# Kernel optimization log

Measured on AMD Instinct MI355X. Metric: run time of the kernel, lower is better.

## Reference

```python
import jax, jax.numpy as jnp
import numpy as np

E = 8          # num_global_experts
K = 2          # top-k
D = 1024       # model_dim
H = 4096       # hidden_size_per_expert
CAP_FACTOR = 1.0


def setup_inputs() -> dict:
    key = jax.random.key(0)
    ks = jax.random.split(key, 5)
    x = jax.random.normal(ks[0], (4, 2048, D), jnp.float32)
    gate_w = jax.random.normal(ks[1], (E, D), jnp.float32) * 0.02
    fc1_w = jax.random.normal(ks[2], (E, H, D), jnp.float32) * 0.02
    fc1_b = jnp.zeros((E, 1, H), jnp.float32)
    fc2_w = jax.random.normal(ks[3], (E, H, D), jnp.float32) * 0.02
    fc2_b = jnp.zeros((E, 1, D), jnp.float32)
    return {"x": x, "gate_w": gate_w, "fc1_w": fc1_w, "fc1_b": fc1_b,
            "fc2_w": fc2_w, "fc2_b": fc2_b}


def reference(x, gate_w, fc1_w, fc1_b, fc2_w, fc2_b):
    B, S, Dm = x.shape
    xf = x.reshape(-1, Dm)                       # [N, D] tokens
    N = xf.shape[0]
    cap = int(K * CAP_FACTOR * ((N + E - 1) // E))  # expert capacity

    # ---- gating (top-k softmax, normalized) ----
    logits = xf @ gate_w.T                       # [N, E]
    scores = jax.nn.softmax(logits, axis=-1)
    topv, topi = jax.lax.top_k(scores, K)        # [N, K]
    gates = topv / jnp.sum(topv, axis=-1, keepdims=True)

    # ---- per-slot locations within each expert (sequential over K slots) ----
    offset = jnp.zeros((E,), jnp.int32)
    locs = []
    for j in range(K):
        mask = jax.nn.one_hot(topi[:, j], E, dtype=jnp.int32)   # [N, E]
        loc_in = jnp.cumsum(mask, axis=0) - 1 + offset[None, :]
        locs.append(jnp.take_along_axis(loc_in, topi[:, j:j + 1], axis=1)[:, 0])
        offset = offset + mask.sum(axis=0)
    loc = jnp.stack(locs, axis=1)                # [N, K]
    valid = loc < cap                            # capacity-dropped tokens
    flat_idx = jnp.where(valid, topi * cap + loc, 0)   # [N, K]
    w = valid.astype(xf.dtype)

    # ---- dispatch (scatter tokens into [E, cap, D], postscore => unweighted) ----
    disp = jnp.zeros((E * cap, Dm), xf.dtype)
    disp = disp.at[flat_idx.reshape(-1)].add(
        (xf[:, None, :] * w[:, :, None]).reshape(-1, Dm))
    de = disp.reshape(E, cap, Dm)

    # ---- batched expert FFN: relu(x @ fc1^T + b1) @ fc2 + b2 ----
    h = jax.nn.relu(jnp.einsum('ecd,ehd->ech', de, fc1_w) + fc1_b)
    eo = jnp.einsum('ech,ehd->ecd', h, fc2_w) + fc2_b

    # ---- combine (gather + gate-weighted sum over K slots) ----
    gathered = eo.reshape(E * cap, Dm)[flat_idx]       # [N, K, D]
    out = jnp.sum(gathered * (gates * w)[:, :, None], axis=1)
    return out.reshape(B, S, Dm)
```

## Files before the change

### kernel.cpp

```cpp
#include <hip/hip_runtime.h>
#include <hip/hip_bf16.h>
#include <stdint.h>

#define NEXP 8
#define DM   1024
#define HID  4096
#define NTOK 8192
#define CAPS 2048

#define BM 256
#define BN 256
#define BK 64

typedef __attribute__((ext_vector_type(8))) short bh8_t;
typedef __attribute__((ext_vector_type(4))) float f32x4_t;
typedef unsigned short u16;

static __device__ __forceinline__ u16 f2bf(float f) {
    __hip_bfloat16 h = __float2bfloat16(f);
    return __builtin_bit_cast(u16, h);
}
static __device__ __forceinline__ float bf2f(u16 u) {
    unsigned int x = ((unsigned int)u) << 16;
    return __builtin_bit_cast(float, x);
}

#define FENCE asm volatile("" ::: "memory")
#define BAR   do { FENCE; __builtin_amdgcn_s_barrier(); FENCE; } while (0)
#define SB0   __builtin_amdgcn_sched_barrier(0)
#define MFMA(d, a, b) d = __builtin_amdgcn_mfma_f32_16x16x32_bf16(a, b, d, 0, 0, 0)

__global__ __launch_bounds__(256) void k_conv_bf16(const float* __restrict__ in,
                                                   u16* __restrict__ out, long n4) {
    long stride = (long)gridDim.x * 256;
    for (long i = (long)blockIdx.x * 256 + threadIdx.x; i < n4; i += stride) {
        float4 v = ((const float4*)in)[i];
        ushort4 o;
        o.x = f2bf(v.x); o.y = f2bf(v.y); o.z = f2bf(v.z); o.w = f2bf(v.w);
        ((ushort4*)out)[i] = o;
    }
}

__global__ __launch_bounds__(256) void k_transpose_w2(const float* __restrict__ in,
                                                      u16* __restrict__ out) {
    int e = blockIdx.z;
    const float* I = in + (long)e * HID * DM;
    u16* O = out + (long)e * DM * HID;
    __shared__ float t[64][65];
    int h0 = blockIdx.x * 64, d0 = blockIdx.y * 64;
    int tid = threadIdx.x;
    int r = tid >> 4, cw = (tid & 15) * 4;
    #pragma unroll
    for (int i = 0; i < 4; ++i) {
        float4 v = *(const float4*)(I + (long)(h0 + r + 16*i) * DM + d0 + cw);
        t[r + 16*i][cw]     = v.x;
        t[r + 16*i][cw + 1] = v.y;
        t[r + 16*i][cw + 2] = v.z;
        t[r + 16*i][cw + 3] = v.w;
    }
    __syncthreads();
    int dl = tid >> 2, hc = (tid & 3) * 16;
    bh8_t w0, w1;
    #pragma unroll
    for (int j = 0; j < 8; ++j) w0[j] = (short)f2bf(t[hc + j][dl]);
    #pragma unroll
    for (int j = 0; j < 8; ++j) w1[j] = (short)f2bf(t[hc + 8 + j][dl]);
    u16* o = O + (long)(d0 + dl) * HID + h0 + hc;
    *(bh8_t*)o = w0;
    *(bh8_t*)(o + 8) = w1;
}

__global__ __launch_bounds__(256) void k_gating(const float* __restrict__ x,
        const float* __restrict__ gw, int* __restrict__ topi, float* __restrict__ gates) {
    __shared__ float sg[NEXP][DM];
    int tid = threadIdx.x;
    for (int i = tid; i < NEXP*DM; i += 256) ((float*)sg)[i] = gw[i];
    __syncthreads();
    int lane = tid & 63, w = tid >> 6;
    long n = (long)blockIdx.x * 4 + w;
    const float* xr = x + n * DM;
    float acc[NEXP] = {};
    for (int i = 0; i < DM/64; ++i) {
        float xv = xr[lane + i*64];
        #pragma unroll
        for (int e = 0; e < NEXP; ++e) acc[e] += xv * sg[e][lane + i*64];
    }
    #pragma unroll
    for (int e = 0; e < NEXP; ++e)
        #pragma unroll
        for (int off = 32; off; off >>= 1) acc[e] += __shfl_xor(acc[e], off);
    if (lane == 0) {
        float mx = acc[0];
        #pragma unroll
        for (int e = 1; e < NEXP; ++e) mx = fmaxf(mx, acc[e]);
        float p[NEXP];
        #pragma unroll
        for (int e = 0; e < NEXP; ++e) p[e] = expf(acc[e] - mx);
        float v0 = p[0]; int i0 = 0;
        #pragma unroll
        for (int e = 1; e < NEXP; ++e) if (p[e] > v0) { v0 = p[e]; i0 = e; }
        float v1 = -1.f; int i1 = 0;
        #pragma unroll
        for (int e = 0; e < NEXP; ++e) if (e != i0 && p[e] > v1) { v1 = p[e]; i1 = e; }
        float tot = v0 + v1;
        topi[n*2]   = i0; topi[n*2+1] = i1;
        gates[n*2]  = v0 / tot; gates[n*2+1] = v1 / tot;
    }
}

__global__ __launch_bounds__(256) void k_locate(const int* __restrict__ topi,
                                                int* __restrict__ flat) {
    __shared__ int st[NTOK * 2];
    __shared__ int wsum[4];
    int tid = threadIdx.x, lane = tid & 63, w = tid >> 6;
    int4* st4 = (int4*)st;
    const int4* g4 = (const int4*)topi;
    for (int i = tid; i < NTOK * 2 / 4; i += 256) st4[i] = g4[i];
    __syncthreads();
    const int TPL = NTOK / 256;
    int base = tid * TPL;
    int offset[NEXP];
    #pragma unroll
    for (int e = 0; e < NEXP; ++e) offset[e] = 0;
    for (int j = 0; j < 2; ++j) {
        unsigned long long pk = 0;
        for (int t = 0; t < TPL; ++t) pk += 1ull << (8 * st[(base + t) * 2 + j]);
        int excl[NEXP];
        #pragma unroll
        for (int e = 0; e < NEXP; ++e) {
            int cnt = (int)((pk >> (8 * e)) & 0xff);
            int v = cnt;
            #pragma unroll
            for (int d = 1; d < 64; d <<= 1) {
                int o = __shfl_up(v, d);
                if (lane >= d) v += o;
            }
            if (lane == 63) wsum[w] = v;
            __syncthreads();
            int wb = 0;
            #pragma unroll
            for (int ww = 0; ww < 4; ++ww) if (ww < w) wb += wsum[ww];
            int tot = wsum[0] + wsum[1] + wsum[2] + wsum[3];
            excl[e] = v - cnt + wb + offset[e];
            offset[e] += tot;
            __syncthreads();
        }
        unsigned long long lo = 0, hi = 0;
        #pragma unroll
        for (int e = 0; e < 4; ++e)    lo |= (unsigned long long)(excl[e] & 0xffff) << (16*e);
        #pragma unroll
        for (int e = 4; e < NEXP; ++e) hi |= (unsigned long long)(excl[e] & 0xffff) << (16*(e-4));
        for (int t = 0; t < TPL; ++t) {
            int n = base + t;
            int e = st[n * 2 + j];
            int sh = 16 * (e & 3);
            int loc;
            if (e < 4) { loc = (int)((lo >> sh) & 0xffff); lo += 1ull << sh; }
            else       { loc = (int)((hi >> sh) & 0xffff); hi += 1ull << sh; }
            st[n * 2 + j] = (loc < CAPS) ? (e * CAPS + loc) : -1;
        }
        __syncthreads();
    }
    int4* f4 = (int4*)flat;
    for (int i = tid; i < NTOK * 2 / 4; i += 256) f4[i] = st4[i];
}

__global__ __launch_bounds__(256) void k_dispatch(const float* __restrict__ x,
        const int* __restrict__ flat, u16* __restrict__ disp) {
    long n = blockIdx.x;
    int tid = threadIdx.x;
    float4 v = *(const float4*)(x + n*DM + tid*4);
    ushort4 o; o.x = f2bf(v.x); o.y = f2bf(v.y); o.z = f2bf(v.z); o.w = f2bf(v.w);
    int f0 = flat[n*2], f1 = flat[n*2+1];
    if (f0 >= 0) *(ushort4*)(disp + (long)f0*DM + tid*4) = o;
    if (f1 >= 0) *(ushort4*)(disp + (long)f1*DM + tid*4) = o;
}

static __device__ __forceinline__ void stage_half(const u16* __restrict__ g, int ld,
                                                  u16* R, int wid, int lane) {
    int rlo = wid*8 + (lane >> 3);
    int cbe = ((lane & 7) ^ ((lane >> 3) & 7)) * 8;
    const u16* s0 = g + (long)rlo * ld + cbe;
    const u16* s1 = g + (long)(rlo + 64) * ld + cbe;
    u16* d0 = R + wid*512 + lane*8;
    u16* d1 = R + 4096 + wid*512 + lane*8;
    __builtin_amdgcn_global_load_lds((const __attribute__((address_space(1))) void*)s0,
        (__attribute__((address_space(3))) void*)d0, 16, 0, 0);
    __builtin_amdgcn_global_load_lds((const __attribute__((address_space(1))) void*)s1,
        (__attribute__((address_space(3))) void*)d1, 16, 0, 0);
}

template<int RELU>
__global__ __launch_bounds__(512, 2)
void k_gemm8(const u16* __restrict__ A, const u16* __restrict__ B,
             const float* __restrict__ bias, u16* __restrict__ C,
             int N, int K, long strA, long strB, long strBias, long strC)
{
    __shared__ u16 sm[2][2][2][8192];

    int gx = gridDim.x, gy = gridDim.y;
    int nwg = gx * gy * (int)gridDim.z;
    int lin = blockIdx.x + gx * (blockIdx.y + gy * blockIdx.z);
    int qq  = nwg >> 3;
    int swz = (lin & 7) * qq + (lin >> 3);
    int gxy = gx * gy;
    int bz = swz / gxy, rm = swz % gxy, by = rm / gx, bx = rm % gx;

    const float* bi = bias + (long)bz * strBias;
    u16* Ce = C + (long)bz * strC;

    long tm = (long)by * BM, tn = (long)bx * BN;
    const u16* Abase = A + (long)bz * strA + tm * (long)K;
    const u16* Bbase = B + (long)bz * strB + tn * (long)K;

    int tid = threadIdx.x, lane = tid & 63, wid = tid >> 6;
    int wr = wid >> 2, wc = wid & 3;

    int frow = lane & 15;
    int fc0 = (((lane >> 4) * 16)      ^ ((lane & 7) << 4)) >> 1;
    int fc1 = ((64 + (lane >> 4) * 16) ^ ((lane & 7) << 4)) >> 1;

    const int NT = K / BK;

    f32x4_t acc[8][4] = {};

    auto STG = [&](int buf, int ab, int half, int kt) {
        const u16* g = (ab ? Bbase : Abase) + (long)(half * 128) * K + (long)kt * BK;
        stage_half(g, K, &sm[buf][ab][half][0], wid, lane);
    };
    auto LDA = [&](int c, int mi, int kk) -> bh8_t {
        const u16* p = &sm[c][0][wr][0] + (mi * 16 + frow) * 64 + (kk ? fc1 : fc0);
        return *(const bh8_t*)p;
    };
    auto LDB = [&](int c, int ni, int kk) -> bh8_t {
        const u16* p = &sm[c][1][wc >> 1][0] + ((wc & 1) * 64 + ni * 16 + frow) * 64 + (kk ? fc1 : fc0);
        return *(const bh8_t*)p;
    };

    auto ktile = [&](int c, int kt, int s12, int s34, int vm) {
        bh8_t a0[4][2], a1[4][2], bf[4][2];
        #pragma unroll
        for (int mi = 0; mi < 4; ++mi) { a0[mi][0] = LDA(c, mi, 0); a0[mi][1] = LDA(c, mi, 1); }
        #pragma unroll
        for (int ni = 0; ni < 2; ++ni) { bf[ni][0] = LDB(c, ni, 0); bf[ni][1] = LDB(c, ni, 1); }
        if (s12) STG(c ^ 1, 0, 1, kt + 1);
        BAR;
        __builtin_amdgcn_s_setprio(1);
        #pragma unroll
        for (int mi = 0; mi < 4; ++mi)
            #pragma unroll
            for (int ni = 0; ni < 2; ++ni)
                #pragma unroll
                for (int kk = 0; kk < 2; ++kk) MFMA(acc[mi][ni], a0[mi][kk], bf[ni][kk]);
        __builtin_amdgcn_s_setprio(0); SB0; BAR;
        #pragma unroll
        for (int ni = 2; ni < 4; ++ni) { bf[ni][0] = LDB(c, ni, 0); bf[ni][1] = LDB(c, ni, 1); }
        if (s12) STG(c ^ 1, 1, 1, kt + 1);
        BAR;
        __builtin_amdgcn_s_setprio(1);
        #pragma unroll
        for (int mi = 0; mi < 4; ++mi)
            #pragma unroll
            for (int ni = 2; ni < 4; ++ni)
                #pragma unroll
                for (int kk = 0; kk < 2; ++kk) MFMA(acc[mi][ni], a0[mi][kk], bf[ni][kk]);
        __builtin_amdgcn_s_setprio(0); SB0; BAR;
        #pragma unroll
        for (int mi = 0; mi < 4; ++mi) { a1[mi][0] = LDA(c, mi + 4, 0); a1[mi][1] = LDA(c, mi + 4, 1); }
        if (s34) STG(c, 1, 0, kt + 2);
        BAR;
        __builtin_amdgcn_s_setprio(1);
        #pragma unroll
        for (int mi = 0; mi < 4; ++mi)
            #pragma unroll
            for (int ni = 0; ni < 2; ++ni)
                #pragma unroll
                for (int kk = 0; kk < 2; ++kk) MFMA(acc[mi + 4][ni], a1[mi][kk], bf[ni][kk]);
        __builtin_amdgcn_s_setprio(0); SB0; BAR;
        if (s34) STG(c, 0, 0, kt + 2);
        BAR;
        __builtin_amdgcn_s_setprio(1);
        #pragma unroll
        for (int mi = 0; mi < 4; ++mi)
            #pragma unroll
            for (int ni = 2; ni < 4; ++ni)
                #pragma unroll
                for (int kk = 0; kk < 2; ++kk) MFMA(acc[mi + 4][ni], a1[mi][kk], bf[ni][kk]);
        __builtin_amdgcn_s_setprio(0); SB0;
        if (vm == 4)      { asm volatile("s_waitcnt vmcnt(4)" ::: "memory"); }
        else if (vm == 0) { asm volatile("s_waitcnt vmcnt(0)" ::: "memory"); }
        BAR;
    };

    STG(0, 0, 0, 0); STG(0, 0, 1, 0); STG(0, 1, 0, 0); STG(0, 1, 1, 0);
    STG(1, 1, 0, 1); STG(1, 0, 0, 1);
    asm volatile("s_waitcnt vmcnt(4)" ::: "memory");
    BAR;

    int kt = 0;
    for (; kt < NT - 2; ++kt) ktile(kt & 1, kt, 1, 1, 4);
    ktile(kt & 1, kt, 1, 0, 0); ++kt;
    ktile(kt & 1, kt, 0, 0, -1);

    u16* wb = &sm[0][0][0][0] + wid * 8192;
    #pragma unroll
    for (int mi = 0; mi < 8; ++mi)
        #pragma unroll
        for (int ni = 0; ni < 4; ++ni) {
            float bv = bi[tn + wc * 64 + ni * 16 + (lane & 15)];
            #pragma unroll
            for (int r = 0; r < 4; ++r) {
                int row = mi * 16 + (lane >> 4) * 4 + r;
                int ce  = ni * 16 + (lane & 15);
                float v = acc[mi][ni][r] + bv;
                if (RELU) v = fmaxf(v, 0.f);
                wb[row * 64 + (ce ^ ((row & 7) << 3))] = f2bf(v);
            }
        }
    __syncthreads();
    long crow = tm + wr * 128;
    long ccol = tn + wc * 64 + (lane & 7) * 8;
    #pragma unroll
    for (int i = 0; i < 16; ++i) {
        int rr = i * 8 + (lane >> 3);
        bh8_t v = *(const bh8_t*)(wb + rr * 64 + (((lane & 7) * 8) ^ ((rr & 7) << 3)));
        *(bh8_t*)(Ce + (crow + rr) * N + ccol) = v;
    }
}

__global__ __launch_bounds__(256) void k_combine(const u16* __restrict__ eo,
        const int* __restrict__ flat, const float* __restrict__ gates,
        float* __restrict__ out) {
    long n = blockIdx.x;
    int tid = threadIdx.x;
    int f0 = flat[n*2], f1 = flat[n*2+1];
    float g0 = (f0 >= 0) ? gates[n*2]   : 0.f;
    float g1 = (f1 >= 0) ? gates[n*2+1] : 0.f;
    const u16* r0 = eo + (long)(f0 >= 0 ? f0 : 0) * DM;
    const u16* r1 = eo + (long)(f1 >= 0 ? f1 : 0) * DM;
    ushort4 a = *(const ushort4*)(r0 + tid*4);
    ushort4 b = *(const ushort4*)(r1 + tid*4);
    float4 o;
    o.x = g0*bf2f(a.x) + g1*bf2f(b.x);
    o.y = g0*bf2f(a.y) + g1*bf2f(b.y);
    o.z = g0*bf2f(a.z) + g1*bf2f(b.z);
    o.w = g0*bf2f(a.w) + g1*bf2f(b.w);
    *(float4*)(out + n*DM + tid*4) = o;
}

extern "C" void kernel_launch(void* const* d_in, const int* in_sizes, int n_in,
                              void* d_out, int out_size, void* d_ws, size_t ws_size,
                              hipStream_t stream) {
    const float* x    = (const float*)d_in[0];
    const float* gw   = (const float*)d_in[1];
    const float* fc1w = (const float*)d_in[2];
    const float* fc1b = (const float*)d_in[3];
    const float* fc2w = (const float*)d_in[4];
    const float* fc2b = (const float*)d_in[5];
    float* out = (float*)d_out;
    char* ws = (char*)d_ws;

    u16* disp = (u16*)(ws);
    u16* eo   = disp;
    u16* h    = (u16*)(ws + 33554432L);
    u16* w1b  = (u16*)(ws + 33554432L + 134217728L);
    u16* w2t  = (u16*)(ws + 33554432L + 134217728L + 67108864L);
    char* tail = ws + 33554432L + 134217728L + 67108864L + 67108864L;
    int*   topi  = (int*)tail;
    float* gates = (float*)(tail + 65536);
    int*   flat  = (int*)(tail + 131072);

    long n1 = (long)NEXP * HID * DM;

    k_conv_bf16<<<dim3(2048), 256, 0, stream>>>(fc1w, w1b, n1 / 4);
    k_transpose_w2<<<dim3(HID/64, DM/64, NEXP), 256, 0, stream>>>(fc2w, w2t);
    k_gating<<<dim3(NTOK/4), 256, 0, stream>>>(x, gw, topi, gates);
    k_locate<<<dim3(1), 256, 0, stream>>>(topi, flat);
    k_dispatch<<<dim3(NTOK), 256, 0, stream>>>(x, flat, disp);
    k_gemm8<1><<<dim3(HID/BN, CAPS/BM, NEXP), 512, 0, stream>>>(
        disp, w1b, fc1b, h, HID, DM,
        (long)CAPS*DM, (long)HID*DM, (long)HID, (long)CAPS*HID);
    k_gemm8<0><<<dim3(DM/BN, CAPS/BM, NEXP), 512, 0, stream>>>(
        h, w2t, fc2b, eo, DM, HID,
        (long)CAPS*HID, (long)DM*HID, (long)DM, (long)CAPS*DM);
    k_combine<<<dim3(NTOK), 256, 0, stream>>>(eo, flat, gates, out);
}
```

Measured before the change: 397.5 us.

## Interleave warp tile ownership across staged halves to pipeline loads finer

Remaps each wave's 128x64 output subtile so it spans both staged halves of A and B (64 rows from each A half, 32 columns from each B half). Each k-tile's four MFMA phases can then start on the first half-tile while the other halves are still loading. The prefetch order and the vmcnt waits are restaged with finer per-phase counts. The epilogue bias indexing and global store addressing are rewritten to match the new fragment mapping. The cost is more complex index math and a different LDS access pattern that may change bank behaviour.

```diff
diff --git a/kernel.cpp b/kernel.cpp
--- a/kernel.cpp
+++ b/kernel.cpp
@@ -29,6 +29,10 @@
 #define BAR   do { FENCE; __builtin_amdgcn_s_barrier(); FENCE; } while (0)
 #define SB0   __builtin_amdgcn_sched_barrier(0)
 #define MFMA(d, a, b) d = __builtin_amdgcn_mfma_f32_16x16x32_bf16(a, b, d, 0, 0, 0)
+#define WAITVM(n) do { if ((n) == 8) asm volatile("s_waitcnt vmcnt(8)" ::: "memory"); \
+    else if ((n) == 4) asm volatile("s_waitcnt vmcnt(4)" ::: "memory"); \
+    else if ((n) == 2) asm volatile("s_waitcnt vmcnt(2)" ::: "memory"); \
+    else if ((n) == 0) asm volatile("s_waitcnt vmcnt(0)" ::: "memory"); } while (0)
 
 __global__ __launch_bounds__(256) void k_conv_bf16(const float* __restrict__ in,
                                                    u16* __restrict__ out, long n4) {
@@ -228,21 +232,34 @@
         const u16* g = (ab ? Bbase : Abase) + (long)(half * 128) * K + (long)kt * BK;
         stage_half(g, K, &sm[buf][ab][half][0], wid, lane);
     };
-    auto LDA = [&](int c, int mi, int kk) -> bh8_t {
-        const u16* p = &sm[c][0][wr][0] + (mi * 16 + frow) * 64 + (kk ? fc1 : fc0);
+    auto LDA = [&](int c, int half, int mi, int kk) -> bh8_t {
+        const u16* p = &sm[c][0][half][0] + (wr * 64 + mi * 16 + frow) * 64 + (kk ? fc1 : fc0);
         return *(const bh8_t*)p;
     };
-    auto LDB = [&](int c, int ni, int kk) -> bh8_t {
-        const u16* p = &sm[c][1][wc >> 1][0] + ((wc & 1) * 64 + ni * 16 + frow) * 64 + (kk ? fc1 : fc0);
+    auto LDB = [&](int c, int half, int ni, int kk) -> bh8_t {
+        const u16* p = &sm[c][1][half][0] + (wc * 32 + ni * 16 + frow) * 64 + (kk ? fc1 : fc0);
         return *(const bh8_t*)p;
     };
 
-    auto ktile = [&](int c, int kt, int s12, int s34, int vm) {
-        bh8_t a0[4][2], a1[4][2], bf[4][2];
-        #pragma unroll
-        for (int mi = 0; mi < 4; ++mi) { a0[mi][0] = LDA(c, mi, 0); a0[mi][1] = LDA(c, mi, 1); }
-        #pragma unroll
-        for (int ni = 0; ni < 2; ++ni) { bf[ni][0] = LDB(c, ni, 0); bf[ni][1] = LDB(c, ni, 1); }
+    auto ktile = [&](int c, int kt, int s12, int s34, int vm1, int vm2, int vm4) {
+        bh8_t a0[4][2], a1[4][2], b0[2][2], b1[2][2];
+        #pragma unroll
+        for (int mi = 0; mi < 4; ++mi) { a0[mi][0] = LDA(c, 0, mi, 0); a0[mi][1] = LDA(c, 0, mi, 1); }
+        #pragma unroll
+        for (int ni = 0; ni < 2; ++ni) { b0[ni][0] = LDB(c, 0, ni, 0); b0[ni][1] = LDB(c, 0, ni, 1); }
+        if (s12) STG(c ^ 1, 1, 1, kt + 1);
+        BAR;
+        __builtin_amdgcn_s_setprio(1);
+        #pragma unroll
+        for (int mi = 0; mi < 4; ++mi)
+            #pragma unroll
+            for (int ni = 0; ni < 2; ++ni)
+                #pragma unroll
+                for (int kk = 0; kk < 2; ++kk) MFMA(acc[mi][ni], a0[mi][kk], b0[ni][kk]);
+        __builtin_amdgcn_s_setprio(0); SB0;
+        WAITVM(vm1); BAR;
+        #pragma unroll
+        for (int ni = 0; ni < 2; ++ni) { b1[ni][0] = LDB(c, 1, ni, 0); b1[ni][1] = LDB(c, 1, ni, 1); }
         if (s12) STG(c ^ 1, 0, 1, kt + 1);
         BAR;
         __builtin_amdgcn_s_setprio(1);
@@ -251,22 +268,21 @@
             #pragma unroll
             for (int ni = 0; ni < 2; ++ni)
                 #pragma unroll
-                for (int kk = 0; kk < 2; ++kk) MFMA(acc[mi][ni], a0[mi][kk], bf[ni][kk]);
-        __builtin_amdgcn_s_setprio(0); SB0; BAR;
-        #pragma unroll
-        for (int ni = 2; ni < 4; ++ni) { bf[ni][0] = LDB(c, ni, 0); bf[ni][1] = LDB(c, ni, 1); }
-        if (s12) STG(c ^ 1, 1, 1, kt + 1);
+                for (int kk = 0; kk < 2; ++kk) MFMA(acc[mi][2 + ni], a0[mi][kk], b1[ni][kk]);
+        __builtin_amdgcn_s_setprio(0); SB0;
+        WAITVM(vm2); BAR;
+        #pragma unroll
+        for (int mi = 0; mi < 4; ++mi) { a1[mi][0] = LDA(c, 1, mi, 0); a1[mi][1] = LDA(c, 1, mi, 1); }
+        if (s34) STG(c, 0, 0, kt + 2);
         BAR;
         __builtin_amdgcn_s_setprio(1);
         #pragma unroll
         for (int mi = 0; mi < 4; ++mi)
             #pragma unroll
-            for (int ni = 2; ni < 4; ++ni)
+            for (int ni = 0; ni < 2; ++ni)
                 #pragma unroll
-                for (int kk = 0; kk < 2; ++kk) MFMA(acc[mi][ni], a0[mi][kk], bf[ni][kk]);
+                for (int kk = 0; kk < 2; ++kk) MFMA(acc[4 + mi][ni], a1[mi][kk], b0[ni][kk]);
         __builtin_amdgcn_s_setprio(0); SB0; BAR;
-        #pragma unroll
-        for (int mi = 0; mi < 4; ++mi) { a1[mi][0] = LDA(c, mi + 4, 0); a1[mi][1] = LDA(c, mi + 4, 1); }
         if (s34) STG(c, 1, 0, kt + 2);
         BAR;
         __builtin_amdgcn_s_setprio(1);
@@ -275,39 +291,27 @@
             #pragma unroll
             for (int ni = 0; ni < 2; ++ni)
                 #pragma unroll
-                for (int kk = 0; kk < 2; ++kk) MFMA(acc[mi + 4][ni], a1[mi][kk], bf[ni][kk]);
-        __builtin_amdgcn_s_setprio(0); SB0; BAR;
-        if (s34) STG(c, 0, 0, kt + 2);
-        BAR;
-        __builtin_amdgcn_s_setprio(1);
-        #pragma unroll
-        for (int mi = 0; mi < 4; ++mi)
-            #pragma unroll
-            for (int ni = 2; ni < 4; ++ni)
-                #pragma unroll
-                for (int kk = 0; kk < 2; ++kk) MFMA(acc[mi + 4][ni], a1[mi][kk], bf[ni][kk]);
+                for (int kk = 0; kk < 2; ++kk) MFMA(acc[4 + mi][2 + ni], a1[mi][kk], b1[ni][kk]);
         __builtin_amdgcn_s_setprio(0); SB0;
-        if (vm == 4)      { asm volatile("s_waitcnt vmcnt(4)" ::: "memory"); }
-        else if (vm == 0) { asm volatile("s_waitcnt vmcnt(0)" ::: "memory"); }
-        BAR;
+        WAITVM(vm4); BAR;
     };
 
-    STG(0, 0, 0, 0); STG(0, 0, 1, 0); STG(0, 1, 0, 0); STG(0, 1, 1, 0);
-    STG(1, 1, 0, 1); STG(1, 0, 0, 1);
+    STG(0, 0, 0, 0); STG(0, 1, 0, 0); STG(0, 1, 1, 0); STG(0, 0, 1, 0);
+    STG(1, 0, 0, 1); STG(1, 1, 0, 1);
     asm volatile("s_waitcnt vmcnt(4)" ::: "memory");
     BAR;
 
     int kt = 0;
-    for (; kt < NT - 2; ++kt) ktile(kt & 1, kt, 1, 1, 4);
-    ktile(kt & 1, kt, 1, 0, 0); ++kt;
-    ktile(kt & 1, kt, 0, 0, -1);
+    for (; kt < NT - 2; ++kt) ktile(kt & 1, kt, 1, 1, 8, 8, 8);
+    ktile(kt & 1, kt, 1, 0, 8, 8, 4); ++kt;
+    ktile(kt & 1, kt, 0, 0, 2, 0, -1);
 
     u16* wb = &sm[0][0][0][0] + wid * 8192;
     #pragma unroll
     for (int mi = 0; mi < 8; ++mi)
         #pragma unroll
         for (int ni = 0; ni < 4; ++ni) {
-            float bv = bi[tn + wc * 64 + ni * 16 + (lane & 15)];
+            float bv = bi[tn + (ni >> 1) * 128 + wc * 32 + (ni & 1) * 16 + (lane & 15)];
             #pragma unroll
             for (int r = 0; r < 4; ++r) {
                 int row = mi * 16 + (lane >> 4) * 4 + r;
@@ -318,13 +322,14 @@
             }
         }
     __syncthreads();
-    long crow = tm + wr * 128;
-    long ccol = tn + wc * 64 + (lane & 7) * 8;
+    long crow0 = tm + wr * 64;
+    long ccol  = tn + wc * 32 + (lane & 3) * 8 + ((lane >> 2) & 1) * 128;
     #pragma unroll
     for (int i = 0; i < 16; ++i) {
         int rr = i * 8 + (lane >> 3);
         bh8_t v = *(const bh8_t*)(wb + rr * 64 + (((lane & 7) * 8) ^ ((rr & 7) << 3)));
-        *(bh8_t*)(Ce + (crow + rr) * N + ccol) = v;
+        long grow = crow0 + (rr & 63) + (rr >> 6) * 128;
+        *(bh8_t*)(Ce + grow * N + ccol) = v;
     }
 }
 
```

Result: no change. 399.8 us (+0.6%).
